# Performance work log

Hardware: AMD Instinct MI355X
Metric: run time of the kernel (lower is better)

## Reference

```python
import jax, jax.numpy as jnp
import numpy as np

C, CL = 64, 8
N_PTS, GRID = 250_000, 160
G2 = GRID // 2


def _build():
    """Build sparse coords and MinkowskiEngine-style kernel maps (numpy, int constants)."""
    rng = np.random.default_rng(0)
    raw = rng.integers(0, GRID, size=(int(N_PTS * 1.3), 3))
    keys = (raw[:, 0] * GRID + raw[:, 1]) * GRID + raw[:, 2]
    _, uidx = np.unique(keys, return_index=True)
    coords = raw[np.sort(uidx)][:N_PTS]
    n_in = coords.shape[0]
    # conv1: kernel 2, stride 2 -> each input voxel maps to exactly one output via one of 8 offsets
    down = coords // 2
    dkeys = (down[:, 0] * G2 + down[:, 1]) * G2 + down[:, 2]
    ukeys, inv = np.unique(dkeys, return_inverse=True)
    n_out = int(ukeys.shape[0])
    kid = (coords[:, 0] % 2) * 4 + (coords[:, 1] % 2) * 2 + (coords[:, 2] % 2)
    lists = [np.where(kid == k)[0] for k in range(8)]
    M1 = max(len(l) for l in lists)
    in1 = np.full((8, M1), n_in, np.int32)   # pad -> zero feature row
    out1 = np.full((8, M1), n_out, np.int32)  # pad -> dropped output row
    for k, l in enumerate(lists):
        in1[k, :len(l)] = l
        out1[k, :len(l)] = inv[l]
    # kernel-3, stride-1 map on the downsampled coordinate set (27 offsets)
    D = np.stack([ukeys // (G2 * G2), (ukeys // G2) % G2, ukeys % G2], 1)
    offs = [(a, b, c) for a in (-1, 0, 1) for b in (-1, 0, 1) for c in (-1, 0, 1)]
    pin, pout = [], []
    for o in offs:
        nd = D + np.array(o)
        valid = np.all((nd >= 0) & (nd < G2), 1)
        nk = (nd[:, 0] * G2 + nd[:, 1]) * G2 + nd[:, 2]
        pos = np.minimum(np.searchsorted(ukeys, nk), n_out - 1)
        found = valid & (ukeys[pos] == nk)
        ii = np.where(found)[0]
        pin.append(ii)
        pout.append(pos[ii])
    M3 = max(len(p) for p in pin)
    in3 = np.full((27, M3), n_out, np.int32)
    out3 = np.full((27, M3), n_out, np.int32)
    for k in range(27):
        in3[k, :len(pin[k])] = pin[k]
        out3[k, :len(pin[k])] = pout[k]
    return n_in, n_out, in1, out1, in3, out3


def setup_inputs() -> dict:
    n_in, n_out, in1, out1, in3, out3 = _build()
    key = jax.random.key(0)
    ks = jax.random.split(key, 16)
    s = 0.05
    return dict(
        x_F=jax.random.normal(ks[0], (n_in, C), jnp.float32),
        ctx_F=jax.random.normal(ks[1], (n_in, C), jnp.float32),
        W1=jax.random.normal(ks[2], (8, 2 * C, C), jnp.float32) * s,
        b1=jax.random.normal(ks[3], (C,), jnp.float32) * s,
        Wr00=jax.random.normal(ks[4], (27, C, C // 4), jnp.float32) * s,
        br00=jax.random.normal(ks[5], (C // 4,), jnp.float32) * s,
        Wr01=jax.random.normal(ks[6], (27, C // 4, C // 2), jnp.float32) * s,
        br01=jax.random.normal(ks[7], (C // 2,), jnp.float32) * s,
        Wr10=jax.random.normal(ks[8], (C, C // 4), jnp.float32) * s,
        br10=jax.random.normal(ks[9], (C // 4,), jnp.float32) * s,
        Wr11=jax.random.normal(ks[10], (27, C // 4, C // 4), jnp.float32) * s,
        br11=jax.random.normal(ks[11], (C // 4,), jnp.float32) * s,
        Wr12=jax.random.normal(ks[12], (C // 4, C // 2), jnp.float32) * s,
        br12=jax.random.normal(ks[13], (C // 2,), jnp.float32) * s,
        W2=jax.random.normal(ks[14], (27, C, CL), jnp.float32) * s,
        b2=jax.random.normal(ks[15], (CL,), jnp.float32) * s,
        in1=jnp.asarray(in1), out1=jnp.asarray(out1),
        in3=jnp.asarray(in3), out3=jnp.asarray(out3),
        n_out=n_out,
    )


def _sconv(F, W, b, in_idx, out_idx, n_out):
    """Kernel-map sparse conv: per-offset gather -> GEMM -> scatter-add. F:[N,Cin], W:[K,Cin,Cout]."""
    Fp = jnp.concatenate([F, jnp.zeros((1, F.shape[1]), F.dtype)], 0)
    y = jnp.zeros((n_out + 1, W.shape[2]), F.dtype)
    for k in range(W.shape[0]):  # fixed small kernel volume (8 or 27)
        y = y.at[out_idx[k]].add(Fp[in_idx[k]] @ W[k])
    return y[:n_out] + b


def reference(x_F, ctx_F, W1, b1, Wr00, br00, Wr01, br01, Wr10, br10, Wr11, br11, Wr12, br12, W2, b2, in1, out1, in3, out3, n_out):
    relu = jax.nn.relu
    f = jnp.concatenate([x_F, ctx_F], 1)               # cat(x.F, context1.F)
    h = _sconv(f, W1, b1, in1, out1, n_out)            # conv1: 2C->C, k=2, s=2
    # InceptionResNet block (PCGCv2-style)
    out0 = _sconv(relu(_sconv(h, Wr00, br00, in3, out3, n_out)), Wr01, br01, in3, out3, n_out)
    t = relu(h @ Wr10 + br10)                          # 1x1 conv
    t = relu(_sconv(t, Wr11, br11, in3, out3, n_out))  # 3x3 conv
    path1 = t @ Wr12 + br12                            # 1x1 conv
    h = jnp.concatenate([out0, path1], 1) + h          # cat + residual
    return _sconv(h, W2, b2, in3, out3, n_out)         # conv2: C->CL, k=3, s=1
```

## Files before the change

kernel.cpp:

```cpp
#include <hip/hip_runtime.h>

#define DEV __device__ __forceinline__

typedef __attribute__((ext_vector_type(8))) short bf16x8;
typedef __attribute__((ext_vector_type(4))) float f32x4;

DEV float4 ld4(const float* p){ return *reinterpret_cast<const float4*>(p); }

DEV unsigned short f2bf(float f){
    union { float f; unsigned u; } v; v.f = f;
    unsigned r = v.u + 0x7fffu + ((v.u >> 16) & 1u);
    return (unsigned short)(r >> 16);
}
DEV float bf2f(unsigned short s){
    union { unsigned u; float f; } v; v.u = ((unsigned)s) << 16;
    return v.f;
}

DEV void async16(const void* g, void* l){
    __builtin_amdgcn_global_load_lds(
        (const __attribute__((address_space(1))) unsigned*)g,
        (__attribute__((address_space(3))) unsigned*)l, 16, 0, 0);
}

#define SB __builtin_amdgcn_sched_barrier(0)

DEV int xcd_swizzle(int orig, int nwg){
    int q = nwg >> 3, r = nwg & 7;
    int x = orig & 7, i = orig >> 3;
    return (x < r ? x*(q+1) : r*(q+1) + (x-r)*q) + i;
}

__global__ __launch_bounds__(256)
void inv_init(int* __restrict__ inv, long n, int defv){
    long i = (long)blockIdx.x*256 + threadIdx.x;
    if (i < n) inv[i] = defv;
}

__global__ __launch_bounds__(256)
void inv_build(const int* __restrict__ inK, const int* __restrict__ outK,
               int* __restrict__ inv, int M, int n_out){
    int k = blockIdx.y;
    int m = blockIdx.x*256 + threadIdx.x;
    if (m >= M) return;
    int o = outK[(long)k*M + m];
    if (o != n_out) inv[(long)k*n_out + o] = inK[(long)k*M + m];
}

__global__ __launch_bounds__(256)
void zero_rows(unsigned short* A, unsigned short* B, unsigned short* C,
               unsigned short* D, unsigned short* E, int n_out){
    int t = threadIdx.x;
    if (t < 64)       A[(long)n_out*64 + t] = 0;
    else if (t < 80)  B[(long)n_out*16 + (t-64)] = 0;
    else if (t < 144) C[(long)n_out*64 + (t-80)] = 0;
    else if (t < 160) D[(long)n_out*16 + (t-144)] = 0;
    else if (t < 176) E[(long)n_out*16 + (t-160)] = 0;
}

__global__ __launch_bounds__(256)
void fill_bias_bf16(unsigned short* __restrict__ A, const float* __restrict__ b, long total){
    long i = (long)blockIdx.x*256 + threadIdx.x;
    if (i < total) A[i] = f2bf(b[i & 63]);
}

__global__ __launch_bounds__(256)
void wfrag_unpaired(const float* __restrict__ W, unsigned short* __restrict__ F,
                    int KC, int NT, int CIN, int CR, int total){
    int idx = blockIdx.x*256 + threadIdx.x;
    if (idx >= total) return;
    int j = idx & 7, l = (idx >> 3) & 63, rest = idx >> 9;
    int nt = rest % NT, cc = rest / NT;
    int k = cc / KC, kc = cc % KC;
    int g = l >> 4, c = l & 15;
    int cin = kc*32 + g*8 + j, cout = nt*16 + c;
    float v = (cout < CR) ? W[((long)k*CIN + cin)*CR + cout] : 0.f;
    F[idx] = f2bf(v);
}

__global__ __launch_bounds__(256)
void wfrag_paired(const float* __restrict__ W, unsigned short* __restrict__ F,
                  int NKr, int NT, int CR, int total){
    int idx = blockIdx.x*256 + threadIdx.x;
    if (idx >= total) return;
    int j = idx & 7, l = (idx >> 3) & 63, rest = idx >> 9;
    int nt = rest % NT, cc = rest / NT;
    int g = l >> 4, c = l & 15;
    int koff = 2*cc + (g >> 1);
    int cin = (g & 1)*8 + j, cout = nt*16 + c;
    float v = (koff < NKr && cout < CR) ? W[((long)koff*16 + cin)*CR + cout] : 0.f;
    F[idx] = f2bf(v);
}

template<bool RELU, bool OUTBF16, int YS, int CR>
__global__ __launch_bounds__(256)
void gather27_lds(const void* __restrict__ Xv, const unsigned short* __restrict__ Wf,
                  const int* __restrict__ inv, const float* __restrict__ bias,
                  void* __restrict__ Yv, int n_out)
{
    __shared__ alignas(16) char buf[3*8192];
    const int lane = threadIdx.x & 63, w = threadIdx.x >> 6;
    const int bid = xcd_swizzle(blockIdx.x, gridDim.x);
    const long jblock = (long)bid * 64;
    if (jblock >= n_out) return;
    const int r = lane & 15, g = lane >> 4;
    const char* X = (const char*)Xv;
    const bf16x8* __restrict__ WF = (const bf16x8*)Wf;

    const int  scol = (((lane & 7) ^ (lane >> 3)) << 4);
    const long jr0 = min(jblock + w*16 +     (lane >> 3), (long)n_out - 1);
    const long jr1 = min(jblock + w*16 + 8 + (lane >> 3), (long)n_out - 1);

    const int rd0 = w*2048 + r*128 + (( 0 + g*16) ^ ((r & 7) << 4));
    const int rd1 = w*2048 + r*128 + ((64 + g*16) ^ ((r & 7) << 4));

    f32x4 acc = {0,0,0,0};

    int p0 = inv[jr0],               p1 = inv[jr1];
    int q0 = inv[(long)n_out + jr0], q1 = inv[(long)n_out + jr1];
    SB;
    async16(X + (long)p0*128 + scol, buf + w*2048);
    async16(X + (long)p1*128 + scol, buf + w*2048 + 1024);
    SB;
    int n0 = inv[(long)2*n_out + jr0], n1 = inv[(long)2*n_out + jr1];
    SB;
    bf16x8 wc0 = WF[lane], wc1 = WF[64 + lane];
    SB;
    async16(X + (long)q0*128 + scol, buf + 8192 + w*2048);
    async16(X + (long)q1*128 + scol, buf + 8192 + w*2048 + 1024);
    SB;
    int m0 = inv[(long)3*n_out + jr0], m1 = inv[(long)3*n_out + jr1];
    SB;
    bf16x8 wd0 = WF[2*64 + lane], wd1 = WF[3*64 + lane];
    SB;

    int cb = 0, db = 2;
    #pragma unroll 1
    for (int k = 0; k < 27; ++k){
        asm volatile("s_waitcnt vmcnt(10)" ::: "memory");
        SB;
        bf16x8 a0 = *(const bf16x8*)(buf + cb*8192 + rd0);
        bf16x8 a1 = *(const bf16x8*)(buf + cb*8192 + rd1);
        SB;
        async16(X + (long)n0*128 + scol, buf + db*8192 + w*2048);
        async16(X + (long)n1*128 + scol, buf + db*8192 + w*2048 + 1024);
        SB;
        const long ki = (long)min(k+4, 26) * n_out;
        int t0 = inv[ki + jr0], t1 = inv[ki + jr1];
        SB;
        const long kw = (long)min(k+2, 26) * 2;
        bf16x8 wn0 = WF[kw*64 + lane], wn1 = WF[(kw+1)*64 + lane];
        SB;
        acc = __builtin_amdgcn_mfma_f32_16x16x32_bf16(a0, wc0, acc, 0, 0, 0);
        acc = __builtin_amdgcn_mfma_f32_16x16x32_bf16(a1, wc1, acc, 0, 0, 0);
        n0 = m0; n1 = m1; m0 = t0; m1 = t1;
        wc0 = wd0; wc1 = wd1; wd0 = wn0; wd1 = wn1;
        cb = (cb == 2) ? 0 : cb + 1;
        db = (db == 2) ? 0 : db + 1;
    }

    const float bv = (r < CR) ? bias[r] : 0.f;
    #pragma unroll
    for (int q = 0; q < 4; ++q){
        long row = jblock + w*16 + g*4 + q;
        if (row < n_out){
            float v = acc[q] + bv;
            if constexpr (RELU) v = fmaxf(v, 0.f);
            if constexpr (OUTBF16) ((unsigned short*)Yv)[row*YS + r] = f2bf(v);
            else if (r < CR)       ((float*)Yv)[row*YS + r] = v;
        }
    }
}

__global__ __launch_bounds__(256)
void conv1_pass(const float* __restrict__ xF, const float* __restrict__ cF,
                const unsigned short* __restrict__ Wfk,
                const int* __restrict__ in1k, const int* __restrict__ out1k,
                unsigned short* __restrict__ A, int M1, int n_in, int n_out)
{
    const int lane = threadIdx.x & 63, wave = threadIdx.x >> 6;
    const int m0 = (blockIdx.x*4 + wave)*16;
    if (m0 >= M1) return;
    const int r = lane & 15, g = lane >> 4;
    const int mc = min(m0 + r, M1-1);
    const int i = in1k[mc];
    const bool valid = i < n_in;
    const long iv = valid ? i : 0;
    const bf16x8* __restrict__ WF = (const bf16x8*)Wfk;
    const bf16x8 az = {0,0,0,0,0,0,0,0};
    f32x4 acc[4];
    #pragma unroll
    for (int nt=0; nt<4; ++nt) acc[nt] = f32x4{0,0,0,0};

    #pragma unroll
    for (int kc=0; kc<4; ++kc){
        const float* s = (kc < 2) ? (xF + iv*64 + kc*32 + g*8)
                                  : (cF + iv*64 + (kc-2)*32 + g*8);
        float4 lo = ld4(s), hi = ld4(s+4);
        bf16x8 a;
        a[0]=(short)f2bf(lo.x); a[1]=(short)f2bf(lo.y);
        a[2]=(short)f2bf(lo.z); a[3]=(short)f2bf(lo.w);
        a[4]=(short)f2bf(hi.x); a[5]=(short)f2bf(hi.y);
        a[6]=(short)f2bf(hi.z); a[7]=(short)f2bf(hi.w);
        if (!valid) a = az;
        #pragma unroll
        for (int nt=0; nt<4; ++nt){
            bf16x8 wv = WF[((long)kc*4 + nt)*64 + lane];
            acc[nt] = __builtin_amdgcn_mfma_f32_16x16x32_bf16(a, wv, acc[nt], 0, 0, 0);
        }
    }

    #pragma unroll
    for (int q=0; q<4; ++q){
        int m = m0 + g*4 + q;
        if (m < M1){
            int o = out1k[m];
            long row = (o == n_out) ? (long)n_out + 1 : (long)o;
            #pragma unroll
            for (int nt=0; nt<4; ++nt){
                long off = row*64 + nt*16 + r;
                A[off] = f2bf(acc[nt][q] + bf2f(A[off]));
            }
        }
    }
}

template<int NK, int G, int NT, int RB, bool RELU, int RESBASE,
         int YS, int CB, int CR, int WPE>
__global__ __launch_bounds__(256, WPE)
void mfma_g1(const void* __restrict__ Xv, const unsigned short* __restrict__ Wf,
             const int* __restrict__ inv, const float* __restrict__ bias,
             const unsigned short* __restrict__ RES, unsigned short* __restrict__ Y, int n_out)
{
    const int lane = threadIdx.x & 63, wave = threadIdx.x >> 6;
    const int jbase = (blockIdx.x*4 + wave)*32;
    if (jbase >= n_out) return;
    const int r = lane & 15, g = lane >> 4;
    const int jc0 = min(jbase + r, n_out-1), jc1 = min(jbase + 16 + r, n_out-1);
    const char* X = (const char*)Xv;
    const bf16x8* __restrict__ WF = (const bf16x8*)Wf;
    f32x4 acc0[NT], acc1[NT];
    #pragma unroll
    for (int nt=0; nt<NT; ++nt){ acc0[nt] = f32x4{0,0,0,0}; acc1[nt] = f32x4{0,0,0,0}; }

    #pragma unroll 1
    for (int g0 = 0; g0 < NK; g0 += G) {
        int b0[G], b1[G];
        #pragma unroll
        for (int kk=0; kk<G; ++kk){
            int koff = 2*(g0+kk) + (g >> 1);
            b0[kk] = inv[(long)koff*n_out + jc0];
            b1[kk] = inv[(long)koff*n_out + jc1];
        }
        #pragma unroll
        for (int kk=0; kk<G; ++kk){
            const int k = g0 + kk;
            bf16x8 a0 = *(const bf16x8*)(X + (long)b0[kk]*RB + (g&1)*16);
            bf16x8 a1 = *(const bf16x8*)(X + (long)b1[kk]*RB + (g&1)*16);
            #pragma unroll
            for (int nt=0; nt<NT; ++nt){
                bf16x8 wv = WF[((long)k*NT + nt)*64 + lane];
                acc0[nt] = __builtin_amdgcn_mfma_f32_16x16x32_bf16(a0, wv, acc0[nt], 0, 0, 0);
                acc1[nt] = __builtin_amdgcn_mfma_f32_16x16x32_bf16(a1, wv, acc1[nt], 0, 0, 0);
            }
        }
    }

    float bi[NT];
    #pragma unroll
    for (int nt=0; nt<NT; ++nt){
        int c = nt*16 + r;
        bi[nt] = (c < CR) ? bias[c] : 0.f;
    }
    #pragma unroll
    for (int q=0; q<4; ++q){
        int row = jbase + g*4 + q;
        if (row < n_out){
            #pragma unroll
            for (int nt=0; nt<NT; ++nt){
                int c = nt*16 + r;
                float v = acc0[nt][q] + bi[nt];
                if constexpr (RESBASE >= 0) v += bf2f(RES[(long)row*64 + RESBASE + c]);
                if constexpr (RELU) v = fmaxf(v, 0.f);
                Y[(long)row*YS + CB + c] = f2bf(v);
            }
        }
        int row2 = jbase + 16 + g*4 + q;
        if (row2 < n_out){
            #pragma unroll
            for (int nt=0; nt<NT; ++nt){
                int c = nt*16 + r;
                float v = acc1[nt][q] + bi[nt];
                if constexpr (RESBASE >= 0) v += bf2f(RES[(long)row2*64 + RESBASE + c]);
                if constexpr (RELU) v = fmaxf(v, 0.f);
                Y[(long)row2*YS + CB + c] = f2bf(v);
            }
        }
    }
}

template<int MODE, int NT, int RB, bool RELU, int RESBASE, int YS, int CB, int CR>
__global__ __launch_bounds__(256)
void mfma_dense(const void* __restrict__ Xv, const unsigned short* __restrict__ Wf,
                const float* __restrict__ bias, const unsigned short* __restrict__ RES,
                unsigned short* __restrict__ Y, int n_out)
{
    const int lane = threadIdx.x & 63, wave = threadIdx.x >> 6;
    const int jbase = (blockIdx.x*4 + wave)*16;
    if (jbase >= n_out) return;
    const int r = lane & 15, g = lane >> 4;
    const int jrow = jbase + r;
    const bool rowok = jrow < n_out;
    const char* X = (const char*)Xv;
    const bf16x8* __restrict__ WF = (const bf16x8*)Wf;
    const bf16x8 az = {0,0,0,0,0,0,0,0};
    f32x4 acc[NT];
    #pragma unroll
    for (int nt=0; nt<NT; ++nt) acc[nt] = f32x4{0,0,0,0};

    if constexpr (MODE == 2) {
        #pragma unroll
        for (int kc=0; kc<2; ++kc){
            bf16x8 a = az;
            if (rowok) a = *(const bf16x8*)(X + (long)jrow*RB + kc*64 + g*16);
            #pragma unroll
            for (int nt=0; nt<NT; ++nt){
                bf16x8 wv = WF[((long)kc*NT + nt)*64 + lane];
                acc[nt] = __builtin_amdgcn_mfma_f32_16x16x32_bf16(a, wv, acc[nt], 0, 0, 0);
            }
        }
    } else {
        bf16x8 a = az;
        if (rowok && g < 2) a = *(const bf16x8*)(X + (long)jrow*RB + (g&1)*16);
        #pragma unroll
        for (int nt=0; nt<NT; ++nt){
            bf16x8 wv = WF[nt*64 + lane];
            acc[nt] = __builtin_amdgcn_mfma_f32_16x16x32_bf16(a, wv, acc[nt], 0, 0, 0);
        }
    }

    float bi[NT];
    #pragma unroll
    for (int nt=0; nt<NT; ++nt){
        int c = nt*16 + r;
        bi[nt] = (c < CR) ? bias[c] : 0.f;
    }
    #pragma unroll
    for (int q=0; q<4; ++q){
        int row = jbase + g*4 + q;
        if (row < n_out){
            #pragma unroll
            for (int nt=0; nt<NT; ++nt){
                int c = nt*16 + r;
                float v = acc[nt][q] + bi[nt];
                if constexpr (RESBASE >= 0) v += bf2f(RES[(long)row*64 + RESBASE + c]);
                if constexpr (RELU) v = fmaxf(v, 0.f);
                Y[(long)row*YS + CB + c] = f2bf(v);
            }
        }
    }
}

extern "C" void kernel_launch(void* const* d_in, const int* in_sizes, int n_in_cnt,
                              void* d_out, int out_size, void* d_ws, size_t ws_size,
                              hipStream_t stream)
{
    const float* xF   = (const float*)d_in[0];
    const float* ctxF = (const float*)d_in[1];
    const float* W1   = (const float*)d_in[2];
    const float* b1   = (const float*)d_in[3];
    const float* Wr00 = (const float*)d_in[4];
    const float* br00 = (const float*)d_in[5];
    const float* Wr01 = (const float*)d_in[6];
    const float* br01 = (const float*)d_in[7];
    const float* Wr10 = (const float*)d_in[8];
    const float* br10 = (const float*)d_in[9];
    const float* Wr11 = (const float*)d_in[10];
    const float* br11 = (const float*)d_in[11];
    const float* Wr12 = (const float*)d_in[12];
    const float* br12 = (const float*)d_in[13];
    const float* W2   = (const float*)d_in[14];
    const float* b2   = (const float*)d_in[15];
    const int* in1  = (const int*)d_in[16];
    const int* out1 = (const int*)d_in[17];
    const int* in3  = (const int*)d_in[18];
    const int* out3 = (const int*)d_in[19];

    const int n_out = out_size / 8;
    const int n_in  = in_sizes[0] / 64;
    const int M1 = in_sizes[16] / 8;
    const int M3 = in_sizes[18] / 27;

    char* p = (char*)d_ws;
    int* inv3 = (int*)p;                 p += (size_t)28*n_out*4;
    unsigned short* A = (unsigned short*)p;  p += (size_t)(n_out+2)*64*2;
    unsigned short* B = (unsigned short*)p;  p += (size_t)(n_out+1)*16*2;
    unsigned short* C = (unsigned short*)p;  p += (size_t)(n_out+1)*64*2;
    unsigned short* D = (unsigned short*)p;  p += (size_t)(n_out+1)*16*2;
    unsigned short* E = (unsigned short*)p;  p += (size_t)(n_out+1)*16*2;
    unsigned short* Wf_c1 = (unsigned short*)p;  p += (size_t)32*4*512*2;
    unsigned short* Wf_00 = (unsigned short*)p;  p += (size_t)54*512*2;
    unsigned short* Wf_2  = (unsigned short*)p;  p += (size_t)54*512*2;
    unsigned short* Wf_01 = (unsigned short*)p;  p += (size_t)14*2*512*2;
    unsigned short* Wf_11 = (unsigned short*)p;  p += (size_t)14*512*2;
    unsigned short* Wf_10 = (unsigned short*)p;  p += (size_t)2*512*2;
    unsigned short* Wf_12 = (unsigned short*)p;  p += (size_t)2*512*2;
    float* OUT = (float*)d_out;

    auto cdiv = [](long a, long b){ return (int)((a + b - 1)/b); };

    inv_init<<<cdiv((long)28*n_out,256),256,0,stream>>>(inv3, (long)28*n_out, n_out);
    inv_build<<<dim3(cdiv(M3,256),27),256,0,stream>>>(in3, out3, inv3, M3, n_out);
    zero_rows<<<1,256,0,stream>>>(A, B, C, D, E, n_out);
    fill_bias_bf16<<<cdiv((long)n_out*64,256),256,0,stream>>>(A, b1, (long)n_out*64);

    wfrag_unpaired<<<cdiv(32*4*512,256),256,0,stream>>>(W1,   Wf_c1, 4, 4, 128, 64, 32*4*512);
    wfrag_unpaired<<<cdiv(54*512,256),  256,0,stream>>>(Wr00, Wf_00, 2, 1,  64, 16, 54*512);
    wfrag_unpaired<<<cdiv(54*512,256),  256,0,stream>>>(W2,   Wf_2,  2, 1,  64,  8, 54*512);
    wfrag_unpaired<<<cdiv(2*512,256),   256,0,stream>>>(Wr10, Wf_10, 2, 1,  64, 16, 2*512);
    wfrag_paired  <<<cdiv(14*2*512,256),256,0,stream>>>(Wr01, Wf_01, 27, 2, 32, 14*2*512);
    wfrag_paired  <<<cdiv(14*512,256),  256,0,stream>>>(Wr11, Wf_11, 27, 1, 16, 14*512);
    wfrag_paired  <<<cdiv(2*512,256),   256,0,stream>>>(Wr12, Wf_12,  1, 2, 32, 2*512);

    for (int k=0; k<8; ++k){
        conv1_pass<<<cdiv(M1,64),256,0,stream>>>(
            xF, ctxF, Wf_c1 + (size_t)k*16*512,
            in1 + (size_t)k*M1, out1 + (size_t)k*M1, A, M1, n_in, n_out);
    }

    const int grid_g = cdiv(n_out, 128);
    const int grid_l = cdiv(n_out, 64);
    const int grid_d = cdiv(n_out, 64);

    gather27_lds<true, true, 16, 16>
        <<<grid_l,256,0,stream>>>(A, Wf_00, inv3, br00, B, n_out);
    mfma_dense<2, 1, 128, true, -1, 16, 0, 16>
        <<<grid_d,256,0,stream>>>(A, Wf_10, br10, nullptr, D, n_out);
    mfma_g1<14,7,2, 32, false, 0, 64, 0, 32, 4>
        <<<grid_g,256,0,stream>>>(B, Wf_01, inv3, br01, A, C, n_out);
    mfma_g1<14,7,1, 32, true, -1, 16, 0, 16, 4>
        <<<grid_g,256,0,stream>>>(D, Wf_11, inv3, br11, nullptr, E, n_out);
    mfma_dense<3, 2, 32, false, 32, 64, 32, 32>
        <<<grid_d,256,0,stream>>>(E, Wf_12, br12, A, C, n_out);
    gather27_lds<false, false, 8, 8>
        <<<grid_l,256,0,stream>>>(C, Wf_2, inv3, b2, OUT, n_out);
}
```

Measured before the change: 296.1 us.

## Restructure conv1 as single scatter-free pass plus gather-sum, deepen gather27 pipeline

Conv1 previously launched eight sequential kernels, each doing a read-modify-write of the accumulated bf16 output. It now runs one 2D-grid kernel that writes per-input-point partial products into a buffer Z indexed by input row. A second kernel then gathers those partials through an inverse map and adds the bias, which removes seven launches and the repeated RMW traffic on A. Separately, the gather27 kernel's LDS ring grows from 3 to 5 stages, prefetching 4 offsets ahead and 8 for indices, with the loop unrolled by 5. This costs more LDS per block and more registers, which may reduce occupancy, plus an extra n_in×64 buffer and an extra inverse-map build.

```diff
diff --git a/kernel.cpp b/kernel.cpp
--- a/kernel.cpp
+++ b/kernel.cpp
@@ -49,19 +49,15 @@
 
 __global__ __launch_bounds__(256)
 void zero_rows(unsigned short* A, unsigned short* B, unsigned short* C,
-               unsigned short* D, unsigned short* E, int n_out){
+               unsigned short* D, unsigned short* E, unsigned short* Z,
+               int n_out, int n_in){
     int t = threadIdx.x;
     if (t < 64)       A[(long)n_out*64 + t] = 0;
     else if (t < 80)  B[(long)n_out*16 + (t-64)] = 0;
     else if (t < 144) C[(long)n_out*64 + (t-80)] = 0;
     else if (t < 160) D[(long)n_out*16 + (t-144)] = 0;
     else if (t < 176) E[(long)n_out*16 + (t-160)] = 0;
-}
-
-__global__ __launch_bounds__(256)
-void fill_bias_bf16(unsigned short* __restrict__ A, const float* __restrict__ b, long total){
-    long i = (long)blockIdx.x*256 + threadIdx.x;
-    if (i < total) A[i] = f2bf(b[i & 63]);
+    else if (t < 240) Z[(long)n_in*64 + (t-176)] = 0;
 }
 
 __global__ __launch_bounds__(256)
@@ -98,7 +94,7 @@
                   const int* __restrict__ inv, const float* __restrict__ bias,
                   void* __restrict__ Yv, int n_out)
 {
-    __shared__ alignas(16) char buf[3*8192];
+    __shared__ alignas(16) char buf[5*8192];
     const int lane = threadIdx.x & 63, w = threadIdx.x >> 6;
     const int bid = xcd_swizzle(blockIdx.x, gridDim.x);
     const long jblock = (long)bid * 64;
@@ -110,56 +106,86 @@
     const int  scol = (((lane & 7) ^ (lane >> 3)) << 4);
     const long jr0 = min(jblock + w*16 +     (lane >> 3), (long)n_out - 1);
     const long jr1 = min(jblock + w*16 + 8 + (lane >> 3), (long)n_out - 1);
+    char* dst0 = buf + w*2048;
 
     const int rd0 = w*2048 + r*128 + (( 0 + g*16) ^ ((r & 7) << 4));
     const int rd1 = w*2048 + r*128 + ((64 + g*16) ^ ((r & 7) << 4));
 
     f32x4 acc = {0,0,0,0};
-
-    int p0 = inv[jr0],               p1 = inv[jr1];
-    int q0 = inv[(long)n_out + jr0], q1 = inv[(long)n_out + jr1];
-    SB;
-    async16(X + (long)p0*128 + scol, buf + w*2048);
-    async16(X + (long)p1*128 + scol, buf + w*2048 + 1024);
-    SB;
-    int n0 = inv[(long)2*n_out + jr0], n1 = inv[(long)2*n_out + jr1];
-    SB;
-    bf16x8 wc0 = WF[lane], wc1 = WF[64 + lane];
-    SB;
-    async16(X + (long)q0*128 + scol, buf + 8192 + w*2048);
-    async16(X + (long)q1*128 + scol, buf + 8192 + w*2048 + 1024);
-    SB;
-    int m0 = inv[(long)3*n_out + jr0], m1 = inv[(long)3*n_out + jr1];
-    SB;
-    bf16x8 wd0 = WF[2*64 + lane], wd1 = WF[3*64 + lane];
-    SB;
-
-    int cb = 0, db = 2;
+    const float bv = (r < CR) ? bias[r] : 0.f;
+    SB;
+
+    int t0a = inv[jr0],                 t0b = inv[jr1];
+    int t1a = inv[(long)1*n_out + jr0], t1b = inv[(long)1*n_out + jr1];
+    int t2a = inv[(long)2*n_out + jr0], t2b = inv[(long)2*n_out + jr1];
+    int t3a = inv[(long)3*n_out + jr0], t3b = inv[(long)3*n_out + jr1];
+    asm volatile("s_waitcnt vmcnt(0)" ::: "memory");
+    SB;
+    int p0a,p0b,p1a,p1b,p2a,p2b,p3a,p3b;
+    bf16x8 wa0,wa1,wb0,wb1,wc0,wc1,wd0,wd1;
+    async16(X + (long)t0a*128 + scol, dst0);
+    async16(X + (long)t0b*128 + scol, dst0 + 1024);
+    SB;
+    p0a = inv[(long)4*n_out + jr0]; p0b = inv[(long)4*n_out + jr1];
+    SB;
+    wa0 = WF[0*64 + lane]; wa1 = WF[1*64 + lane];
+    SB;
+    async16(X + (long)t1a*128 + scol, dst0 + 1*8192);
+    async16(X + (long)t1b*128 + scol, dst0 + 1*8192 + 1024);
+    SB;
+    p1a = inv[(long)5*n_out + jr0]; p1b = inv[(long)5*n_out + jr1];
+    SB;
+    wb0 = WF[2*64 + lane]; wb1 = WF[3*64 + lane];
+    SB;
+    async16(X + (long)t2a*128 + scol, dst0 + 2*8192);
+    async16(X + (long)t2b*128 + scol, dst0 + 2*8192 + 1024);
+    SB;
+    p2a = inv[(long)6*n_out + jr0]; p2b = inv[(long)6*n_out + jr1];
+    SB;
+    wc0 = WF[4*64 + lane]; wc1 = WF[5*64 + lane];
+    SB;
+    async16(X + (long)t3a*128 + scol, dst0 + 3*8192);
+    async16(X + (long)t3b*128 + scol, dst0 + 3*8192 + 1024);
+    SB;
+    p3a = inv[(long)7*n_out + jr0]; p3b = inv[(long)7*n_out + jr1];
+    SB;
+    wd0 = WF[6*64 + lane]; wd1 = WF[7*64 + lane];
+    SB;
+
+    #define ITER(KK, CB, DB)                                                          \
+    {                                                                                 \
+        asm volatile("s_waitcnt vmcnt(22)" ::: "memory");                             \
+        SB;                                                                           \
+        bf16x8 a0 = *(const bf16x8*)(buf + (CB)*8192 + rd0);                          \
+        bf16x8 a1 = *(const bf16x8*)(buf + (CB)*8192 + rd1);                          \
+        SB;                                                                           \
+        async16(X + (long)p0a*128 + scol, dst0 + (DB)*8192);                          \
+        async16(X + (long)p0b*128 + scol, dst0 + (DB)*8192 + 1024);                   \
+        SB;                                                                           \
+        const long ki_ = (long)(((KK)+8 < 26) ? (KK)+8 : 26) * n_out;                 \
+        int na_ = inv[ki_ + jr0], nb_ = inv[ki_ + jr1];                               \
+        SB;                                                                           \
+        const long kw_ = (long)(((KK)+4 < 26) ? (KK)+4 : 26) * 2;                     \
+        bf16x8 nw0_ = WF[kw_*64 + lane], nw1_ = WF[(kw_+1)*64 + lane];                \
+        SB;                                                                           \
+        acc = __builtin_amdgcn_mfma_f32_16x16x32_bf16(a0, wa0, acc, 0, 0, 0);         \
+        acc = __builtin_amdgcn_mfma_f32_16x16x32_bf16(a1, wa1, acc, 0, 0, 0);         \
+        p0a=p1a; p0b=p1b; p1a=p2a; p1b=p2b; p2a=p3a; p2b=p3b; p3a=na_; p3b=nb_;       \
+        wa0=wb0; wa1=wb1; wb0=wc0; wb1=wc1; wc0=wd0; wc1=wd1; wd0=nw0_; wd1=nw1_;     \
+    }
+
     #pragma unroll 1
-    for (int k = 0; k < 27; ++k){
-        asm volatile("s_waitcnt vmcnt(10)" ::: "memory");
-        SB;
-        bf16x8 a0 = *(const bf16x8*)(buf + cb*8192 + rd0);
-        bf16x8 a1 = *(const bf16x8*)(buf + cb*8192 + rd1);
-        SB;
-        async16(X + (long)n0*128 + scol, buf + db*8192 + w*2048);
-        async16(X + (long)n1*128 + scol, buf + db*8192 + w*2048 + 1024);
-        SB;
-        const long ki = (long)min(k+4, 26) * n_out;
-        int t0 = inv[ki + jr0], t1 = inv[ki + jr1];
-        SB;
-        const long kw = (long)min(k+2, 26) * 2;
-        bf16x8 wn0 = WF[kw*64 + lane], wn1 = WF[(kw+1)*64 + lane];
-        SB;
-        acc = __builtin_amdgcn_mfma_f32_16x16x32_bf16(a0, wc0, acc, 0, 0, 0);
-        acc = __builtin_amdgcn_mfma_f32_16x16x32_bf16(a1, wc1, acc, 0, 0, 0);
-        n0 = m0; n1 = m1; m0 = t0; m1 = t1;
-        wc0 = wd0; wc1 = wd1; wd0 = wn0; wd1 = wn1;
-        cb = (cb == 2) ? 0 : cb + 1;
-        db = (db == 2) ? 0 : db + 1;
-    }
-
-    const float bv = (r < CR) ? bias[r] : 0.f;
+    for (int k = 0; k < 25; k += 5){
+        ITER(k+0, 0, 4) ITER(k+1, 1, 0) ITER(k+2, 2, 1)
+        ITER(k+3, 3, 2) ITER(k+4, 4, 3)
+    }
+    ITER(25, 0, 4)
+    ITER(26, 1, 0)
+    #undef ITER
+
+    asm volatile("s_waitcnt vmcnt(0)" ::: "memory");
+    SB;
+
     #pragma unroll
     for (int q = 0; q < 4; ++q){
         long row = jblock + w*16 + g*4 + q;
@@ -173,20 +199,21 @@
 }
 
 __global__ __launch_bounds__(256)
-void conv1_pass(const float* __restrict__ xF, const float* __restrict__ cF,
-                const unsigned short* __restrict__ Wfk,
-                const int* __restrict__ in1k, const int* __restrict__ out1k,
-                unsigned short* __restrict__ A, int M1, int n_in, int n_out)
+void conv1_z(const float* __restrict__ xF, const float* __restrict__ cF,
+             const unsigned short* __restrict__ Wfc1, const int* __restrict__ in1,
+             unsigned short* __restrict__ Z, int M1, int n_in)
 {
+    const int k = blockIdx.y;
     const int lane = threadIdx.x & 63, wave = threadIdx.x >> 6;
     const int m0 = (blockIdx.x*4 + wave)*16;
     if (m0 >= M1) return;
     const int r = lane & 15, g = lane >> 4;
+    const int* __restrict__ in1k = in1 + (long)k*M1;
     const int mc = min(m0 + r, M1-1);
     const int i = in1k[mc];
     const bool valid = i < n_in;
     const long iv = valid ? i : 0;
-    const bf16x8* __restrict__ WF = (const bf16x8*)Wfk;
+    const bf16x8* __restrict__ WF = (const bf16x8*)(Wfc1 + (size_t)k*16*512);
     const bf16x8 az = {0,0,0,0,0,0,0,0};
     f32x4 acc[4];
     #pragma unroll
@@ -214,15 +241,42 @@
     for (int q=0; q<4; ++q){
         int m = m0 + g*4 + q;
         if (m < M1){
-            int o = out1k[m];
-            long row = (o == n_out) ? (long)n_out + 1 : (long)o;
+            int oi = in1k[m];
+            long row = (oi < n_in) ? (long)oi : (long)n_in + 1;
             #pragma unroll
-            for (int nt=0; nt<4; ++nt){
-                long off = row*64 + nt*16 + r;
-                A[off] = f2bf(acc[nt][q] + bf2f(A[off]));
-            }
-        }
-    }
+            for (int nt=0; nt<4; ++nt)
+                Z[row*64 + nt*16 + r] = f2bf(acc[nt][q]);
+        }
+    }
+}
+
+__global__ __launch_bounds__(256)
+void conv1_sum(const unsigned short* __restrict__ Z, const int* __restrict__ inv1,
+               const float* __restrict__ b1, unsigned short* __restrict__ A, int n_out)
+{
+    const long t = (long)blockIdx.x*256 + threadIdx.x;
+    const long o = t >> 3;
+    if (o >= n_out) return;
+    const int c8 = (int)(t & 7) * 8;
+    int b[8];
+    #pragma unroll
+    for (int k=0;k<8;++k) b[k] = inv1[(long)k*n_out + o];
+    float acc[8];
+    #pragma unroll
+    for (int j=0;j<2;++j){
+        float4 v = ld4(b1 + c8 + 4*j);
+        acc[4*j]=v.x; acc[4*j+1]=v.y; acc[4*j+2]=v.z; acc[4*j+3]=v.w;
+    }
+    #pragma unroll
+    for (int k=0;k<8;++k){
+        bf16x8 z = *(const bf16x8*)(Z + (long)b[k]*64 + c8);
+        #pragma unroll
+        for (int j=0;j<8;++j) acc[j] += bf2f((unsigned short)z[j]);
+    }
+    bf16x8 outv;
+    #pragma unroll
+    for (int j=0;j<8;++j) outv[j] = (short)f2bf(acc[j]);
+    *(bf16x8*)(A + o*64 + c8) = outv;
 }
 
 template<int NK, int G, int NT, int RB, bool RELU, int RESBASE,
@@ -393,11 +447,13 @@
 
     char* p = (char*)d_ws;
     int* inv3 = (int*)p;                 p += (size_t)28*n_out*4;
-    unsigned short* A = (unsigned short*)p;  p += (size_t)(n_out+2)*64*2;
+    int* inv1 = (int*)p;                 p += (size_t)8*n_out*4;
+    unsigned short* A = (unsigned short*)p;  p += (size_t)(n_out+1)*64*2;
     unsigned short* B = (unsigned short*)p;  p += (size_t)(n_out+1)*16*2;
     unsigned short* C = (unsigned short*)p;  p += (size_t)(n_out+1)*64*2;
     unsigned short* D = (unsigned short*)p;  p += (size_t)(n_out+1)*16*2;
     unsigned short* E = (unsigned short*)p;  p += (size_t)(n_out+1)*16*2;
+    unsigned short* Z = (unsigned short*)p;  p += (size_t)(n_in+2)*64*2;
     unsigned short* Wf_c1 = (unsigned short*)p;  p += (size_t)32*4*512*2;
     unsigned short* Wf_00 = (unsigned short*)p;  p += (size_t)54*512*2;
     unsigned short* Wf_2  = (unsigned short*)p;  p += (size_t)54*512*2;
@@ -410,9 +466,10 @@
     auto cdiv = [](long a, long b){ return (int)((a + b - 1)/b); };
 
     inv_init<<<cdiv((long)28*n_out,256),256,0,stream>>>(inv3, (long)28*n_out, n_out);
+    inv_init<<<cdiv((long)8*n_out,256),256,0,stream>>>(inv1, (long)8*n_out, n_in);
     inv_build<<<dim3(cdiv(M3,256),27),256,0,stream>>>(in3, out3, inv3, M3, n_out);
-    zero_rows<<<1,256,0,stream>>>(A, B, C, D, E, n_out);
-    fill_bias_bf16<<<cdiv((long)n_out*64,256),256,0,stream>>>(A, b1, (long)n_out*64);
+    inv_build<<<dim3(cdiv(M1,256),8),256,0,stream>>>(in1, out1, inv1, M1, n_out);
+    zero_rows<<<1,256,0,stream>>>(A, B, C, D, E, Z, n_out, n_in);
 
     wfrag_unpaired<<<cdiv(32*4*512,256),256,0,stream>>>(W1,   Wf_c1, 4, 4, 128, 64, 32*4*512);
     wfrag_unpaired<<<cdiv(54*512,256),  256,0,stream>>>(Wr00, Wf_00, 2, 1,  64, 16, 54*512);
@@ -422,11 +479,8 @@
     wfrag_paired  <<<cdiv(14*512,256),  256,0,stream>>>(Wr11, Wf_11, 27, 1, 16, 14*512);
     wfrag_paired  <<<cdiv(2*512,256),   256,0,stream>>>(Wr12, Wf_12,  1, 2, 32, 2*512);
 
-    for (int k=0; k<8; ++k){
-        conv1_pass<<<cdiv(M1,64),256,0,stream>>>(
-            xF, ctxF, Wf_c1 + (size_t)k*16*512,
-            in1 + (size_t)k*M1, out1 + (size_t)k*M1, A, M1, n_in, n_out);
-    }
+    conv1_z<<<dim3(cdiv(M1,64),8),256,0,stream>>>(xF, ctxF, Wf_c1, in1, Z, M1, n_in);
+    conv1_sum<<<cdiv((long)8*n_out,256),256,0,stream>>>(Z, inv1, b1, A, n_out);
 
     const int grid_g = cdiv(n_out, 128);
     const int grid_l = cdiv(n_out, 64);
```

After: 280.3 us. 5.3% less time.
